# Kernel optimization log

Measured on AMD Instinct MI355X. Metric: run time of the kernel, lower is better.

Reference implementation:

```python
import jax, jax.numpy as jnp
import numpy as np

B, N, GI, GH, GO = 8, 1024, 1024, 128, 128


def _lin_params(k, din, dout):
    # torch.nn.Linear default init: U(-1/sqrt(din), 1/sqrt(din))
    s = 1.0 / np.sqrt(din)
    kw, kb = jax.random.split(k)
    W = jax.random.uniform(kw, (din, dout), jnp.float32, -s, s)
    b = jax.random.uniform(kb, (dout,), jnp.float32, -s, s)
    return W, b


def setup_inputs() -> dict:
    key = jax.random.key(0)
    ks = jax.random.split(key, 6)
    aa_rep = jax.random.normal(ks[0], (B, N, GI), dtype=jnp.float32)
    rpa = jax.random.randint(ks[1], (B, N, N), 0, 2).astype(jnp.int32)
    W_in, b_in = _lin_params(ks[2], GI, GH)
    W_h0, b_h0 = _lin_params(ks[3], GH, GH)
    W_h1, b_h1 = _lin_params(ks[4], GH, GH)
    W_out, b_out = _lin_params(ks[5], GH, GO)
    return dict(aa_rep=aa_rep, rpa=rpa, W_in=W_in, b_in=b_in,
                W_h0=W_h0, b_h0=b_h0, W_h1=W_h1, b_h1=b_h1,
                W_out=W_out, b_out=b_out)


def _norm_adj(rpa):
    # get_graph_edge: edges = nonzero(rpa) minus self-loops; GCNConv then
    # re-adds self-loops and applies symmetric deg^{-1/2} normalization.
    n = rpa.shape[-1]
    A = (rpa != 0).astype(jnp.float32)
    eye = jnp.eye(n, dtype=jnp.float32)
    A = A * (1.0 - eye) + eye  # [B,N,N] A_hat = A (no diag) + I
    deg = A.sum(-1)  # [B,N], includes self-loop
    dinv = jnp.where(deg > 0, 1.0 / jnp.sqrt(deg), 0.0)
    return A * dinv[..., :, None] * dinv[..., None, :]


def reference(aa_rep, rpa, W_in, b_in, W_h0, b_h0, W_h1, b_h1, W_out, b_out):
    Ahat = _norm_adj(rpa)  # [B,N,N]

    def gcn(h, W, b):
        # GCNConv: aggregate(normalized) of (h @ W), then bias; model applies relu
        return jax.nn.relu(jnp.einsum('bij,bjd->bid', Ahat, h @ W) + b)

    h1 = gcn(aa_rep, W_in, b_in)   # layer_in
    h2 = gcn(h1, W_h0, b_h0)       # hidden 0
    h3 = gcn(h2, W_h1, b_h1)       # hidden 1
    h4 = gcn(h3, W_out, b_out)     # layer_out
    # mean over stacked layer outputs reps[1:]
    return (h1 + h2 + h3 + h4) * 0.25
```

## Files before the change

### kernel.cpp

```cpp
#include <hip/hip_runtime.h>
#include <hip/hip_bf16.h>

typedef __bf16 bf16;
typedef __bf16 bf16x4 __attribute__((ext_vector_type(4)));
typedef __bf16 bf16x8 __attribute__((ext_vector_type(8)));
typedef float f32x4 __attribute__((ext_vector_type(4)));

#define NN 1024
#define GH 128
#define MROWS 8192

static __device__ __forceinline__ f32x4 mfma16(bf16x8 a, bf16x8 b, f32x4 c) {
    return __builtin_amdgcn_mfma_f32_16x16x32_bf16(a, b, c, 0, 0, 0);
}

__global__ __launch_bounds__(256) void prep_kernel(
        const int* __restrict__ rpa,
        const float* __restrict__ W0, const float* __restrict__ W1,
        const float* __restrict__ W2, const float* __restrict__ W3,
        unsigned char* __restrict__ A01b, float* __restrict__ dinv,
        bf16* __restrict__ T0, bf16* __restrict__ T1,
        bf16* __restrict__ T2, bf16* __restrict__ T3) {
    int bid = blockIdx.x;
    {
        int rb = (bid & 7) * 256 + (bid >> 3);
        int row  = rb * 4 + (threadIdx.x >> 6);
        int lane = threadIdx.x & 63;
        int i = row & (NN - 1);
        const int4* p = reinterpret_cast<const int4*>(rpa + (size_t)row * NN);
        unsigned char* brow = A01b + (size_t)row * 128;
        int cnt = 0;
#pragma unroll
        for (int it = 0; it < 4; ++it) {
            int4 v = p[lane + it * 64];
            int j = (lane + it * 64) * 4;
            int a0 = (v.x != 0), a1 = (v.y != 0), a2 = (v.z != 0), a3 = (v.w != 0);
            cnt += (a0 & (j + 0 != i)) + (a1 & (j + 1 != i)) +
                   (a2 & (j + 2 != i)) + (a3 & (j + 3 != i));
            unsigned nib = (unsigned)(a0 | (j + 0 == i))
                         | ((unsigned)(a1 | (j + 1 == i)) << 1)
                         | ((unsigned)(a2 | (j + 2 == i)) << 2)
                         | ((unsigned)(a3 | (j + 3 == i)) << 3);
            unsigned pn = __shfl_xor(nib, 1, 64);
            if (!(lane & 1))
                brow[it * 32 + (lane >> 1)] = (unsigned char)(nib | (pn << 4));
        }
#pragma unroll
        for (int off = 32; off > 0; off >>= 1) cnt += __shfl_down(cnt, off, 64);
        if (lane == 0) dinv[row] = rsqrtf((float)(cnt + 1));
    }
    if (threadIdx.x < 11) {
        int t = bid * 11 + threadIdx.x;
        const float* W; bf16* T; int K; int local;
        if (t < 16384)      { W = W0; T = T0; K = NN; local = t; }
        else if (t < 18432) { W = W1; T = T1; K = GH; local = t - 16384; }
        else if (t < 20480) { W = W2; T = T2; K = GH; local = t - 18432; }
        else                { W = W3; T = T3; K = GH; local = t - 20480; }
        int n = local & 127, k0 = (local >> 7) * 8;
        bf16x8 o;
#pragma unroll
        for (int ii = 0; ii < 8; ++ii) o[ii] = (bf16)W[(size_t)(k0 + ii) * GH + n];
        *reinterpret_cast<bf16x8*>(T + (size_t)n * K + k0) = o;
    }
}

__global__ __launch_bounds__(512, 4) void gemm3_kernel(const float* __restrict__ aa,
                                                       const bf16* __restrict__ Wt,
                                                       const float* __restrict__ dinv,
                                                       bf16* __restrict__ Zt) {
    __shared__ bf16 Alds[32768];
    int tid = threadIdx.x;
    int wave = tid >> 6, lane = tid & 63;
    int lrow = lane & 15, lg = lane >> 4;
    int lb = (blockIdx.x & 7) * 32 + (blockIdx.x >> 3);
    int m0 = lb * 32;
#pragma unroll
    for (int i = 0; i < 8; ++i) {
        int idx = i * 512 + tid;
        int row = idx >> 7, u = idx & 127;
        const float* src = aa + (size_t)(m0 + row) * NN + u * 8;
        float4 f0 = *reinterpret_cast<const float4*>(src);
        float4 f1 = *reinterpret_cast<const float4*>(src + 4);
        bf16x8 v;
        v[0] = (bf16)f0.x; v[1] = (bf16)f0.y; v[2] = (bf16)f0.z; v[3] = (bf16)f0.w;
        v[4] = (bf16)f1.x; v[5] = (bf16)f1.y; v[6] = (bf16)f1.z; v[7] = (bf16)f1.w;
        *reinterpret_cast<bf16x8*>(&Alds[(row * 128 + (u ^ (row & 7))) * 8]) = v;
    }
    __syncthreads();
    int c0 = wave * 16;
    const bf16* Bp = Wt + (size_t)(c0 + lrow) * NN + lg * 8;
    f32x4 acc[2][2] = {};
#pragma unroll
    for (int f = 0; f < 32; ++f) {
        bf16x8 bb = *reinterpret_cast<const bf16x8*>(Bp + f * 32);
        int u = f * 4 + lg;
#pragma unroll
        for (int rg = 0; rg < 2; ++rg) {
            int r = rg * 16 + lrow;
            bf16x8 a = *reinterpret_cast<const bf16x8*>(&Alds[(r * 128 + (u ^ (r & 7))) * 8]);
            acc[rg][f & 1] = mfma16(a, bb, acc[rg][f & 1]);
        }
    }
    int rl = lg * 4;
    int col = c0 + lrow;
#pragma unroll
    for (int rg = 0; rg < 2; ++rg) {
        f32x4 s = acc[rg][0] + acc[rg][1];
        int rbase = m0 + rg * 16 + rl;
        float4 d4 = *reinterpret_cast<const float4*>(&dinv[rbase]);
        bf16x4 o;
        o[0] = (bf16)(s[0] * d4.x);
        o[1] = (bf16)(s[1] * d4.y);
        o[2] = (bf16)(s[2] * d4.z);
        o[3] = (bf16)(s[3] * d4.w);
        *reinterpret_cast<bf16x4*>(Zt + (size_t)col * MROWS + rbase) = o;
    }
}

template <int MODE, bool HASW>
__global__ __launch_bounds__(512, 4) void fused3_kernel(const unsigned char* __restrict__ A01b,
                                                        const bf16* __restrict__ Xt,
                                                        const bf16* __restrict__ Wt,
                                                        const float* __restrict__ dinv,
                                                        const float* __restrict__ bias,
                                                        bf16* __restrict__ Hst,
                                                        float* __restrict__ outp) {
    __shared__ bf16 Alds[16384];
    __shared__ bf16 Ths[4096];
    __shared__ bf16 Tls[4096];
    int tid = threadIdx.x;
    int wave = tid >> 6, lane = tid & 63;
    int lrow = lane & 15, lg = lane >> 4;
    int lb = (blockIdx.x & 7) * 32 + (blockIdx.x >> 3);
    int m0 = lb * 32;
    int b = blockIdx.x & 7;
    int c0 = wave * 16;
    const bf16* Bp = Xt + (size_t)(c0 + lrow) * MROWS + b * NN + lg * 8;
    f32x4 acc[2][2] = {};
    int erow = tid >> 4;
    int eub  = (tid & 15) * 4;
    int ers  = erow & 7;
#pragma unroll
    for (int h = 0; h < 2; ++h) {
        if (h) __syncthreads();
        {
            unsigned w = *reinterpret_cast<const unsigned*>(
                A01b + (size_t)(m0 + erow) * 128 + h * 64 + eub);
#pragma unroll
            for (int i = 0; i < 4; ++i) {
                unsigned byte = (w >> (8 * i)) & 0xffu;
                bf16x8 v;
#pragma unroll
                for (int k = 0; k < 8; ++k) v[k] = ((byte >> k) & 1u) ? (bf16)1.f : (bf16)0.f;
                *reinterpret_cast<bf16x8*>(&Alds[(erow * 64 + ((eub + i) ^ ers)) * 8]) = v;
            }
        }
        __syncthreads();
#pragma unroll
        for (int fl = 0; fl < 16; ++fl) {
            int f = h * 16 + fl;
            bf16x8 bb = *reinterpret_cast<const bf16x8*>(Bp + f * 32);
            int ul = fl * 4 + lg;
#pragma unroll
            for (int rg = 0; rg < 2; ++rg) {
                int r = rg * 16 + lrow;
                bf16x8 a = *reinterpret_cast<const bf16x8*>(&Alds[(r * 64 + (ul ^ (r & 7))) * 8]);
                acc[rg][f & 1] = mfma16(a, bb, acc[rg][f & 1]);
            }
        }
    }
    int rl = lg * 4;

    if constexpr (!HASW) {
#pragma unroll
        for (int rg = 0; rg < 2; ++rg) {
            f32x4 s = acc[rg][0] + acc[rg][1];
            int rbase = m0 + rg * 16 + rl;
            float4 d4 = *reinterpret_cast<const float4*>(&dinv[rbase]);
            int col = c0 + lrow;
            float bv = bias[col];
            float v0 = fmaxf(s[0] * d4.x + bv, 0.f);
            float v1 = fmaxf(s[1] * d4.y + bv, 0.f);
            float v2 = fmaxf(s[2] * d4.z + bv, 0.f);
            float v3 = fmaxf(s[3] * d4.w + bv, 0.f);
            float* op = outp + (size_t)rbase * GH + col;
            if (MODE == 0) {
                op[0] = 0.25f * v0; op[GH] = 0.25f * v1;
                op[2 * GH] = 0.25f * v2; op[3 * GH] = 0.25f * v3;
            } else {
                op[0] += 0.25f * v0; op[GH] += 0.25f * v1;
                op[2 * GH] += 0.25f * v2; op[3 * GH] += 0.25f * v3;
            }
            if (MODE != 2) {
                bf16x4 h4;
                h4[0] = (bf16)(v0 * d4.x); h4[1] = (bf16)(v1 * d4.y);
                h4[2] = (bf16)(v2 * d4.z); h4[3] = (bf16)(v3 * d4.w);
                *reinterpret_cast<bf16x4*>(Hst + (size_t)col * MROWS + rbase) = h4;
            }
        }
    } else {
        __syncthreads();
        {
            int tcol = c0 + lrow;
#pragma unroll
            for (int rg = 0; rg < 2; ++rg) {
                f32x4 s = acc[rg][0] + acc[rg][1];
#pragma unroll
                for (int r = 0; r < 4; ++r) {
                    int trow = rg * 16 + rl + r;
                    float tv = s[r];
                    bf16 hi = (bf16)tv;
                    int ei = trow * 128 + (tcol ^ ((trow & 7) << 3));
                    Ths[ei] = hi;
                    Tls[ei] = (bf16)(tv - (float)hi);
                }
            }
        }
        __syncthreads();
        f32x4 u[2] = {};
        int wcol = c0 + lrow;
#pragma unroll
        for (int ks = 0; ks < 4; ++ks) {
            int e0 = ks * 32 + lg * 8;
            bf16x8 wv = *reinterpret_cast<const bf16x8*>(Wt + (size_t)wcol * GH + e0);
#pragma unroll
            for (int rg = 0; rg < 2; ++rg) {
                int trow2 = rg * 16 + lrow;
                int te = trow2 * 128 + (e0 ^ ((trow2 & 7) << 3));
                bf16x8 thi = *reinterpret_cast<const bf16x8*>(&Ths[te]);
                bf16x8 tlo = *reinterpret_cast<const bf16x8*>(&Tls[te]);
                u[rg] = mfma16(thi, wv, u[rg]);
                u[rg] = mfma16(tlo, wv, u[rg]);
            }
        }
#pragma unroll
        for (int rg = 0; rg < 2; ++rg) {
            int rbase = m0 + rg * 16 + rl;
            float4 d4 = *reinterpret_cast<const float4*>(&dinv[rbase]);
            float bv = bias[wcol];
            float v0 = fmaxf(u[rg][0] * d4.x + bv, 0.f);
            float v1 = fmaxf(u[rg][1] * d4.y + bv, 0.f);
            float v2 = fmaxf(u[rg][2] * d4.z + bv, 0.f);
            float v3 = fmaxf(u[rg][3] * d4.w + bv, 0.f);
            float* op = outp + (size_t)rbase * GH + wcol;
            if (MODE == 0) {
                op[0] = 0.25f * v0; op[GH] = 0.25f * v1;
                op[2 * GH] = 0.25f * v2; op[3 * GH] = 0.25f * v3;
            } else {
                op[0] += 0.25f * v0; op[GH] += 0.25f * v1;
                op[2 * GH] += 0.25f * v2; op[3 * GH] += 0.25f * v3;
            }
            if (MODE != 2) {
                bf16x4 h4;
                h4[0] = (bf16)(v0 * d4.x); h4[1] = (bf16)(v1 * d4.y);
                h4[2] = (bf16)(v2 * d4.z); h4[3] = (bf16)(v3 * d4.w);
                *reinterpret_cast<bf16x4*>(Hst + (size_t)wcol * MROWS + rbase) = h4;
            }
        }
    }
}

extern "C" void kernel_launch(void* const* d_in, const int* in_sizes, int n_in,
                              void* d_out, int out_size, void* d_ws, size_t ws_size,
                              hipStream_t stream) {
    const float* aa    = (const float*)d_in[0];
    const int*   rpa   = (const int*)d_in[1];
    const float* W_in  = (const float*)d_in[2];
    const float* b_in  = (const float*)d_in[3];
    const float* W_h0  = (const float*)d_in[4];
    const float* b_h0  = (const float*)d_in[5];
    const float* W_h1  = (const float*)d_in[6];
    const float* b_h1  = (const float*)d_in[7];
    const float* W_out = (const float*)d_in[8];
    const float* b_out = (const float*)d_in[9];
    float* out = (float*)d_out;

    char* ws = (char*)d_ws;
    size_t off = 0;
    float* dinv = (float*)(ws + off); off += (size_t)MROWS * 4;
    unsigned char* A01b = (unsigned char*)(ws + off); off += (size_t)MROWS * 128;
    bf16*  Xt   = (bf16*)(ws + off);  off += (size_t)GH * MROWS * 2;
    bf16*  HstA = (bf16*)(ws + off);  off += (size_t)GH * MROWS * 2;
    bf16*  HstB = (bf16*)(ws + off);  off += (size_t)GH * MROWS * 2;
    bf16*  Wt0  = (bf16*)(ws + off);  off += (size_t)GH * NN * 2;
    bf16*  Wt1  = (bf16*)(ws + off);  off += (size_t)GH * GH * 2;
    bf16*  Wt2  = (bf16*)(ws + off);  off += (size_t)GH * GH * 2;
    bf16*  Wt3  = (bf16*)(ws + off);  off += (size_t)GH * GH * 2;

    prep_kernel<<<2048, 256, 0, stream>>>(rpa, W_in, W_h0, W_h1, W_out,
                                          A01b, dinv, Wt0, Wt1, Wt2, Wt3);
    gemm3_kernel<<<256, 512, 0, stream>>>(aa, Wt0, dinv, Xt);
    fused3_kernel<0, false><<<256, 512, 0, stream>>>(A01b, Xt,   Wt1, dinv, b_in,  HstA, out);
    fused3_kernel<1, true><<<256, 512, 0, stream>>>(A01b, HstA, Wt1, dinv, b_h0, HstB, out);
    fused3_kernel<1, true><<<256, 512, 0, stream>>>(A01b, HstB, Wt2, dinv, b_h1, HstA, out);
    fused3_kernel<2, true><<<256, 512, 0, stream>>>(A01b, HstA, Wt3, dinv, b_out, HstB, out);
}
```

Measured before the change: 75.60 us.

## Enlarge GEMM and fused aggregation tiles to 64 rows with 1024-thread blocks

Both the input GEMM and the fused aggregation kernels now use 1024-thread blocks covering 64 rows, with two row-halves of 8 waves each sharing the same column B-fragments. The K dimension is staged through LDS in four chunks instead of one or two. The redundant barrier before the transform-scratch writes is removed. This roughly halves global B-operand traffic per row, but the grid drops to 128 blocks, which may leave half the CUs idle and adds more barriers per block.

```diff
diff --git a/kernel.cpp b/kernel.cpp
--- a/kernel.cpp
+++ b/kernel.cpp
@@ -64,41 +64,50 @@
     }
 }
 
-__global__ __launch_bounds__(512, 4) void gemm3_kernel(const float* __restrict__ aa,
-                                                       const bf16* __restrict__ Wt,
-                                                       const float* __restrict__ dinv,
-                                                       bf16* __restrict__ Zt) {
-    __shared__ bf16 Alds[32768];
+__global__ __launch_bounds__(1024, 4) void gemm4_kernel(const float* __restrict__ aa,
+                                                        const bf16* __restrict__ Wt,
+                                                        const float* __restrict__ dinv,
+                                                        bf16* __restrict__ Zt) {
+    __shared__ bf16 Alds[16384];
     int tid = threadIdx.x;
     int wave = tid >> 6, lane = tid & 63;
     int lrow = lane & 15, lg = lane >> 4;
-    int lb = (blockIdx.x & 7) * 32 + (blockIdx.x >> 3);
-    int m0 = lb * 32;
-#pragma unroll
-    for (int i = 0; i < 8; ++i) {
-        int idx = i * 512 + tid;
-        int row = idx >> 7, u = idx & 127;
-        const float* src = aa + (size_t)(m0 + row) * NN + u * 8;
-        float4 f0 = *reinterpret_cast<const float4*>(src);
-        float4 f1 = *reinterpret_cast<const float4*>(src + 4);
-        bf16x8 v;
-        v[0] = (bf16)f0.x; v[1] = (bf16)f0.y; v[2] = (bf16)f0.z; v[3] = (bf16)f0.w;
-        v[4] = (bf16)f1.x; v[5] = (bf16)f1.y; v[6] = (bf16)f1.z; v[7] = (bf16)f1.w;
-        *reinterpret_cast<bf16x8*>(&Alds[(row * 128 + (u ^ (row & 7))) * 8]) = v;
-    }
-    __syncthreads();
-    int c0 = wave * 16;
+    int colg = wave & 7, rowh = wave >> 3;
+    int lb = (blockIdx.x & 7) * 16 + (blockIdx.x >> 3);
+    int m0 = lb * 64;
+    int c0 = colg * 16;
     const bf16* Bp = Wt + (size_t)(c0 + lrow) * NN + lg * 8;
     f32x4 acc[2][2] = {};
-#pragma unroll
-    for (int f = 0; f < 32; ++f) {
-        bf16x8 bb = *reinterpret_cast<const bf16x8*>(Bp + f * 32);
-        int u = f * 4 + lg;
-#pragma unroll
-        for (int rg = 0; rg < 2; ++rg) {
-            int r = rg * 16 + lrow;
-            bf16x8 a = *reinterpret_cast<const bf16x8*>(&Alds[(r * 128 + (u ^ (r & 7))) * 8]);
-            acc[rg][f & 1] = mfma16(a, bb, acc[rg][f & 1]);
+    int arow = tid >> 4;
+    int au   = (tid & 15) * 2;
+    int ars  = arow & 7;
+#pragma unroll
+    for (int h = 0; h < 4; ++h) {
+        if (h) __syncthreads();
+        {
+            const float* src = aa + (size_t)(m0 + arow) * NN + h * 256 + au * 8;
+#pragma unroll
+            for (int i = 0; i < 2; ++i) {
+                float4 f0 = *reinterpret_cast<const float4*>(src + i * 8);
+                float4 f1 = *reinterpret_cast<const float4*>(src + i * 8 + 4);
+                bf16x8 v;
+                v[0] = (bf16)f0.x; v[1] = (bf16)f0.y; v[2] = (bf16)f0.z; v[3] = (bf16)f0.w;
+                v[4] = (bf16)f1.x; v[5] = (bf16)f1.y; v[6] = (bf16)f1.z; v[7] = (bf16)f1.w;
+                *reinterpret_cast<bf16x8*>(&Alds[(arow * 32 + ((au + i) ^ ars)) * 8]) = v;
+            }
+        }
+        __syncthreads();
+#pragma unroll
+        for (int fl = 0; fl < 8; ++fl) {
+            int f = h * 8 + fl;
+            bf16x8 bb = *reinterpret_cast<const bf16x8*>(Bp + f * 32);
+            int ul = fl * 4 + lg;
+#pragma unroll
+            for (int rg = 0; rg < 2; ++rg) {
+                int r = rowh * 32 + rg * 16 + lrow;
+                bf16x8 a = *reinterpret_cast<const bf16x8*>(&Alds[(r * 32 + (ul ^ (r & 7))) * 8]);
+                acc[rg][f & 1] = mfma16(a, bb, acc[rg][f & 1]);
+            }
         }
     }
     int rl = lg * 4;
@@ -106,7 +115,7 @@
 #pragma unroll
     for (int rg = 0; rg < 2; ++rg) {
         f32x4 s = acc[rg][0] + acc[rg][1];
-        int rbase = m0 + rg * 16 + rl;
+        int rbase = m0 + rowh * 32 + rg * 16 + rl;
         float4 d4 = *reinterpret_cast<const float4*>(&dinv[rbase]);
         bf16x4 o;
         o[0] = (bf16)(s[0] * d4.x);
@@ -118,53 +127,54 @@
 }
 
 template <int MODE, bool HASW>
-__global__ __launch_bounds__(512, 4) void fused3_kernel(const unsigned char* __restrict__ A01b,
-                                                        const bf16* __restrict__ Xt,
-                                                        const bf16* __restrict__ Wt,
-                                                        const float* __restrict__ dinv,
-                                                        const float* __restrict__ bias,
-                                                        bf16* __restrict__ Hst,
-                                                        float* __restrict__ outp) {
+__global__ __launch_bounds__(1024, 4) void fused4_kernel(const unsigned char* __restrict__ A01b,
+                                                         const bf16* __restrict__ Xt,
+                                                         const bf16* __restrict__ Wt,
+                                                         const float* __restrict__ dinv,
+                                                         const float* __restrict__ bias,
+                                                         bf16* __restrict__ Hst,
+                                                         float* __restrict__ outp) {
     __shared__ bf16 Alds[16384];
-    __shared__ bf16 Ths[4096];
-    __shared__ bf16 Tls[4096];
+    __shared__ bf16 Ths[8192];
+    __shared__ bf16 Tls[8192];
     int tid = threadIdx.x;
     int wave = tid >> 6, lane = tid & 63;
     int lrow = lane & 15, lg = lane >> 4;
-    int lb = (blockIdx.x & 7) * 32 + (blockIdx.x >> 3);
-    int m0 = lb * 32;
+    int colg = wave & 7, rowh = wave >> 3;
+    int lb = (blockIdx.x & 7) * 16 + (blockIdx.x >> 3);
+    int m0 = lb * 64;
     int b = blockIdx.x & 7;
-    int c0 = wave * 16;
+    int c0 = colg * 16;
     const bf16* Bp = Xt + (size_t)(c0 + lrow) * MROWS + b * NN + lg * 8;
     f32x4 acc[2][2] = {};
     int erow = tid >> 4;
-    int eub  = (tid & 15) * 4;
+    int eu2  = (tid & 15) * 2;
     int ers  = erow & 7;
 #pragma unroll
-    for (int h = 0; h < 2; ++h) {
+    for (int h = 0; h < 4; ++h) {
         if (h) __syncthreads();
         {
-            unsigned w = *reinterpret_cast<const unsigned*>(
-                A01b + (size_t)(m0 + erow) * 128 + h * 64 + eub);
-#pragma unroll
-            for (int i = 0; i < 4; ++i) {
+            unsigned short w = *reinterpret_cast<const unsigned short*>(
+                A01b + (size_t)(m0 + erow) * 128 + h * 32 + eu2);
+#pragma unroll
+            for (int i = 0; i < 2; ++i) {
                 unsigned byte = (w >> (8 * i)) & 0xffu;
                 bf16x8 v;
 #pragma unroll
                 for (int k = 0; k < 8; ++k) v[k] = ((byte >> k) & 1u) ? (bf16)1.f : (bf16)0.f;
-                *reinterpret_cast<bf16x8*>(&Alds[(erow * 64 + ((eub + i) ^ ers)) * 8]) = v;
+                *reinterpret_cast<bf16x8*>(&Alds[(erow * 32 + ((eu2 + i) ^ ers)) * 8]) = v;
             }
         }
         __syncthreads();
 #pragma unroll
-        for (int fl = 0; fl < 16; ++fl) {
-            int f = h * 16 + fl;
+        for (int fl = 0; fl < 8; ++fl) {
+            int f = h * 8 + fl;
             bf16x8 bb = *reinterpret_cast<const bf16x8*>(Bp + f * 32);
             int ul = fl * 4 + lg;
 #pragma unroll
             for (int rg = 0; rg < 2; ++rg) {
-                int r = rg * 16 + lrow;
-                bf16x8 a = *reinterpret_cast<const bf16x8*>(&Alds[(r * 64 + (ul ^ (r & 7))) * 8]);
+                int r = rowh * 32 + rg * 16 + lrow;
+                bf16x8 a = *reinterpret_cast<const bf16x8*>(&Alds[(r * 32 + (ul ^ (r & 7))) * 8]);
                 acc[rg][f & 1] = mfma16(a, bb, acc[rg][f & 1]);
             }
         }
@@ -172,12 +182,12 @@
     int rl = lg * 4;
 
     if constexpr (!HASW) {
+        int col = c0 + lrow;
 #pragma unroll
         for (int rg = 0; rg < 2; ++rg) {
             f32x4 s = acc[rg][0] + acc[rg][1];
-            int rbase = m0 + rg * 16 + rl;
+            int rbase = m0 + rowh * 32 + rg * 16 + rl;
             float4 d4 = *reinterpret_cast<const float4*>(&dinv[rbase]);
-            int col = c0 + lrow;
             float bv = bias[col];
             float v0 = fmaxf(s[0] * d4.x + bv, 0.f);
             float v1 = fmaxf(s[1] * d4.y + bv, 0.f);
@@ -199,7 +209,6 @@
             }
         }
     } else {
-        __syncthreads();
         {
             int tcol = c0 + lrow;
 #pragma unroll
@@ -207,7 +216,7 @@
                 f32x4 s = acc[rg][0] + acc[rg][1];
 #pragma unroll
                 for (int r = 0; r < 4; ++r) {
-                    int trow = rg * 16 + rl + r;
+                    int trow = rowh * 32 + rg * 16 + rl + r;
                     float tv = s[r];
                     bf16 hi = (bf16)tv;
                     int ei = trow * 128 + (tcol ^ ((trow & 7) << 3));
@@ -225,7 +234,7 @@
             bf16x8 wv = *reinterpret_cast<const bf16x8*>(Wt + (size_t)wcol * GH + e0);
 #pragma unroll
             for (int rg = 0; rg < 2; ++rg) {
-                int trow2 = rg * 16 + lrow;
+                int trow2 = rowh * 32 + rg * 16 + lrow;
                 int te = trow2 * 128 + (e0 ^ ((trow2 & 7) << 3));
                 bf16x8 thi = *reinterpret_cast<const bf16x8*>(&Ths[te]);
                 bf16x8 tlo = *reinterpret_cast<const bf16x8*>(&Tls[te]);
@@ -235,7 +244,7 @@
         }
 #pragma unroll
         for (int rg = 0; rg < 2; ++rg) {
-            int rbase = m0 + rg * 16 + rl;
+            int rbase = m0 + rowh * 32 + rg * 16 + rl;
             float4 d4 = *reinterpret_cast<const float4*>(&dinv[rbase]);
             float bv = bias[wcol];
             float v0 = fmaxf(u[rg][0] * d4.x + bv, 0.f);
@@ -289,9 +298,9 @@
 
     prep_kernel<<<2048, 256, 0, stream>>>(rpa, W_in, W_h0, W_h1, W_out,
                                           A01b, dinv, Wt0, Wt1, Wt2, Wt3);
-    gemm3_kernel<<<256, 512, 0, stream>>>(aa, Wt0, dinv, Xt);
-    fused3_kernel<0, false><<<256, 512, 0, stream>>>(A01b, Xt,   Wt1, dinv, b_in,  HstA, out);
-    fused3_kernel<1, true><<<256, 512, 0, stream>>>(A01b, HstA, Wt1, dinv, b_h0, HstB, out);
-    fused3_kernel<1, true><<<256, 512, 0, stream>>>(A01b, HstB, Wt2, dinv, b_h1, HstA, out);
-    fused3_kernel<2, true><<<256, 512, 0, stream>>>(A01b, HstA, Wt3, dinv, b_out, HstB, out);
-}
+    gemm4_kernel<<<128, 1024, 0, stream>>>(aa, Wt0, dinv, Xt);
+    fused4_kernel<0, false><<<128, 1024, 0, stream>>>(A01b, Xt,   Wt1, dinv, b_in,  HstA, out);
+    fused4_kernel<1, true><<<128, 1024, 0, stream>>>(A01b, HstA, Wt1, dinv, b_h0, HstB, out);
+    fused4_kernel<1, true><<<128, 1024, 0, stream>>>(A01b, HstB, Wt2, dinv, b_h1, HstA, out);
+    fused4_kernel<2, true><<<128, 1024, 0, stream>>>(A01b, HstA, Wt3, dinv, b_out, HstB, out);
+}
```

Result: slower. 122.4 us (+61.9%).

## Merge adjacency prep with first GEMM and fold dinv scaling into aggregation

Applied to the files above, without the earlier changes.

Splits the W_in transpose into its own small kernel, then fuses the adjacency bit-packing and degree computation with the aa@W_in GEMM in a single launch. Because the GEMM no longer waits on dinv, the column dinv scaling moves into the first aggregation kernel, where the adjacency tile is built with dinv values instead of ones. This removes one dependency and lets the memory-bound rpa scan overlap with the GEMM. The cost is an extra tiny launch, extra dinv loads in the first aggregation, and a different bf16 rounding point.

```diff
diff --git a/kernel.cpp b/kernel.cpp
--- a/kernel.cpp
+++ b/kernel.cpp
@@ -14,18 +14,29 @@
     return __builtin_amdgcn_mfma_f32_16x16x32_bf16(a, b, c, 0, 0, 0);
 }
 
-__global__ __launch_bounds__(256) void prep_kernel(
-        const int* __restrict__ rpa,
-        const float* __restrict__ W0, const float* __restrict__ W1,
-        const float* __restrict__ W2, const float* __restrict__ W3,
+__global__ __launch_bounds__(256) void wtrans0_kernel(const float* __restrict__ W0,
+                                                      bf16* __restrict__ T0) {
+    int t = blockIdx.x * 256 + threadIdx.x;
+    int n = t & 127, k0 = (t >> 7) * 8;
+    bf16x8 o;
+#pragma unroll
+    for (int ii = 0; ii < 8; ++ii) o[ii] = (bf16)W0[(size_t)(k0 + ii) * GH + n];
+    *reinterpret_cast<bf16x8*>(T0 + (size_t)n * NN + k0) = o;
+}
+
+__global__ __launch_bounds__(512, 4) void prep_gemm_kernel(
+        const int* __restrict__ rpa, const float* __restrict__ aa,
+        const float* __restrict__ W1, const float* __restrict__ W2, const float* __restrict__ W3,
+        const bf16* __restrict__ Wt0,
         unsigned char* __restrict__ A01b, float* __restrict__ dinv,
-        bf16* __restrict__ T0, bf16* __restrict__ T1,
-        bf16* __restrict__ T2, bf16* __restrict__ T3) {
-    int bid = blockIdx.x;
-    {
-        int rb = (bid & 7) * 256 + (bid >> 3);
-        int row  = rb * 4 + (threadIdx.x >> 6);
-        int lane = threadIdx.x & 63;
+        bf16* __restrict__ T1, bf16* __restrict__ T2, bf16* __restrict__ T3,
+        bf16* __restrict__ Yt) {
+    __shared__ bf16 Alds[32768];
+    int bid = blockIdx.x, tid = threadIdx.x;
+    if (bid < 1024) {
+        int rb = (bid & 7) * 128 + (bid >> 3);
+        int wave = tid >> 6, lane = tid & 63;
+        int row = rb * 8 + wave;
         int i = row & (NN - 1);
         const int4* p = reinterpret_cast<const int4*>(rpa + (size_t)row * NN);
         unsigned char* brow = A01b + (size_t)row * 128;
@@ -48,76 +59,65 @@
 #pragma unroll
         for (int off = 32; off > 0; off >>= 1) cnt += __shfl_down(cnt, off, 64);
         if (lane == 0) dinv[row] = rsqrtf((float)(cnt + 1));
+        if (tid < 6) {
+            int t = bid * 6 + tid;
+            const float* W; bf16* T; int local;
+            if (t < 2048)      { W = W1; T = T1; local = t; }
+            else if (t < 4096) { W = W2; T = T2; local = t - 2048; }
+            else               { W = W3; T = T3; local = t - 4096; }
+            int n = local & 127, k0 = (local >> 7) * 8;
+            bf16x8 o;
+#pragma unroll
+            for (int ii = 0; ii < 8; ++ii) o[ii] = (bf16)W[(size_t)(k0 + ii) * GH + n];
+            *reinterpret_cast<bf16x8*>(T + (size_t)n * GH + k0) = o;
+        }
+    } else {
+        int g = bid - 1024;
+        int wave = tid >> 6, lane = tid & 63;
+        int lrow = lane & 15, lg = lane >> 4;
+        int lb = (g & 7) * 32 + (g >> 3);
+        int m0 = lb * 32;
+#pragma unroll
+        for (int i = 0; i < 8; ++i) {
+            int idx = i * 512 + tid;
+            int row = idx >> 7, u = idx & 127;
+            const float* src = aa + (size_t)(m0 + row) * NN + u * 8;
+            float4 f0 = *reinterpret_cast<const float4*>(src);
+            float4 f1 = *reinterpret_cast<const float4*>(src + 4);
+            bf16x8 v;
+            v[0] = (bf16)f0.x; v[1] = (bf16)f0.y; v[2] = (bf16)f0.z; v[3] = (bf16)f0.w;
+            v[4] = (bf16)f1.x; v[5] = (bf16)f1.y; v[6] = (bf16)f1.z; v[7] = (bf16)f1.w;
+            *reinterpret_cast<bf16x8*>(&Alds[(row * 128 + (u ^ (row & 7))) * 8]) = v;
+        }
+        __syncthreads();
+        int c0 = wave * 16;
+        const bf16* Bp = Wt0 + (size_t)(c0 + lrow) * NN + lg * 8;
+        f32x4 acc[2][2] = {};
+#pragma unroll
+        for (int f = 0; f < 32; ++f) {
+            bf16x8 bb = *reinterpret_cast<const bf16x8*>(Bp + f * 32);
+            int u = f * 4 + lg;
+#pragma unroll
+            for (int rg = 0; rg < 2; ++rg) {
+                int r = rg * 16 + lrow;
+                bf16x8 a = *reinterpret_cast<const bf16x8*>(&Alds[(r * 128 + (u ^ (r & 7))) * 8]);
+                acc[rg][f & 1] = mfma16(a, bb, acc[rg][f & 1]);
+            }
+        }
+        int rl = lg * 4;
+        int col = c0 + lrow;
+#pragma unroll
+        for (int rg = 0; rg < 2; ++rg) {
+            f32x4 s = acc[rg][0] + acc[rg][1];
+            int rbase = m0 + rg * 16 + rl;
+            bf16x4 o;
+            o[0] = (bf16)s[0]; o[1] = (bf16)s[1]; o[2] = (bf16)s[2]; o[3] = (bf16)s[3];
+            *reinterpret_cast<bf16x4*>(Yt + (size_t)col * MROWS + rbase) = o;
+        }
     }
-    if (threadIdx.x < 11) {
-        int t = bid * 11 + threadIdx.x;
-        const float* W; bf16* T; int K; int local;
-        if (t < 16384)      { W = W0; T = T0; K = NN; local = t; }
-        else if (t < 18432) { W = W1; T = T1; K = GH; local = t - 16384; }
-        else if (t < 20480) { W = W2; T = T2; K = GH; local = t - 18432; }
-        else                { W = W3; T = T3; K = GH; local = t - 20480; }
-        int n = local & 127, k0 = (local >> 7) * 8;
-        bf16x8 o;
-#pragma unroll
-        for (int ii = 0; ii < 8; ++ii) o[ii] = (bf16)W[(size_t)(k0 + ii) * GH + n];
-        *reinterpret_cast<bf16x8*>(T + (size_t)n * K + k0) = o;
-    }
-}
-
-__global__ __launch_bounds__(512, 4) void gemm3_kernel(const float* __restrict__ aa,
-                                                       const bf16* __restrict__ Wt,
-                                                       const float* __restrict__ dinv,
-                                                       bf16* __restrict__ Zt) {
-    __shared__ bf16 Alds[32768];
-    int tid = threadIdx.x;
-    int wave = tid >> 6, lane = tid & 63;
-    int lrow = lane & 15, lg = lane >> 4;
-    int lb = (blockIdx.x & 7) * 32 + (blockIdx.x >> 3);
-    int m0 = lb * 32;
-#pragma unroll
-    for (int i = 0; i < 8; ++i) {
-        int idx = i * 512 + tid;
-        int row = idx >> 7, u = idx & 127;
-        const float* src = aa + (size_t)(m0 + row) * NN + u * 8;
-        float4 f0 = *reinterpret_cast<const float4*>(src);
-        float4 f1 = *reinterpret_cast<const float4*>(src + 4);
-        bf16x8 v;
-        v[0] = (bf16)f0.x; v[1] = (bf16)f0.y; v[2] = (bf16)f0.z; v[3] = (bf16)f0.w;
-        v[4] = (bf16)f1.x; v[5] = (bf16)f1.y; v[6] = (bf16)f1.z; v[7] = (bf16)f1.w;
-        *reinterpret_cast<bf16x8*>(&Alds[(row * 128 + (u ^ (row & 7))) * 8]) = v;
-    }
-    __syncthreads();
-    int c0 = wave * 16;
-    const bf16* Bp = Wt + (size_t)(c0 + lrow) * NN + lg * 8;
-    f32x4 acc[2][2] = {};
-#pragma unroll
-    for (int f = 0; f < 32; ++f) {
-        bf16x8 bb = *reinterpret_cast<const bf16x8*>(Bp + f * 32);
-        int u = f * 4 + lg;
-#pragma unroll
-        for (int rg = 0; rg < 2; ++rg) {
-            int r = rg * 16 + lrow;
-            bf16x8 a = *reinterpret_cast<const bf16x8*>(&Alds[(r * 128 + (u ^ (r & 7))) * 8]);
-            acc[rg][f & 1] = mfma16(a, bb, acc[rg][f & 1]);
-        }
-    }
-    int rl = lg * 4;
-    int col = c0 + lrow;
-#pragma unroll
-    for (int rg = 0; rg < 2; ++rg) {
-        f32x4 s = acc[rg][0] + acc[rg][1];
-        int rbase = m0 + rg * 16 + rl;
-        float4 d4 = *reinterpret_cast<const float4*>(&dinv[rbase]);
-        bf16x4 o;
-        o[0] = (bf16)(s[0] * d4.x);
-        o[1] = (bf16)(s[1] * d4.y);
-        o[2] = (bf16)(s[2] * d4.z);
-        o[3] = (bf16)(s[3] * d4.w);
-        *reinterpret_cast<bf16x4*>(Zt + (size_t)col * MROWS + rbase) = o;
-    }
-}
-
-template <int MODE, bool HASW>
+}
+
+template <int MODE, bool HASW, bool DSCALE>
 __global__ __launch_bounds__(512, 4) void fused3_kernel(const unsigned char* __restrict__ A01b,
                                                         const bf16* __restrict__ Xt,
                                                         const bf16* __restrict__ Wt,
@@ -150,8 +150,22 @@
             for (int i = 0; i < 4; ++i) {
                 unsigned byte = (w >> (8 * i)) & 0xffu;
                 bf16x8 v;
-#pragma unroll
-                for (int k = 0; k < 8; ++k) v[k] = ((byte >> k) & 1u) ? (bf16)1.f : (bf16)0.f;
+                if constexpr (DSCALE) {
+                    const float* dq = dinv + b * NN + (h * 64 + eub + i) * 8;
+                    float4 q0 = *reinterpret_cast<const float4*>(dq);
+                    float4 q1 = *reinterpret_cast<const float4*>(dq + 4);
+                    v[0] = (byte & 1u)   ? (bf16)q0.x : (bf16)0.f;
+                    v[1] = (byte & 2u)   ? (bf16)q0.y : (bf16)0.f;
+                    v[2] = (byte & 4u)   ? (bf16)q0.z : (bf16)0.f;
+                    v[3] = (byte & 8u)   ? (bf16)q0.w : (bf16)0.f;
+                    v[4] = (byte & 16u)  ? (bf16)q1.x : (bf16)0.f;
+                    v[5] = (byte & 32u)  ? (bf16)q1.y : (bf16)0.f;
+                    v[6] = (byte & 64u)  ? (bf16)q1.z : (bf16)0.f;
+                    v[7] = (byte & 128u) ? (bf16)q1.w : (bf16)0.f;
+                } else {
+#pragma unroll
+                    for (int k = 0; k < 8; ++k) v[k] = ((byte >> k) & 1u) ? (bf16)1.f : (bf16)0.f;
+                }
                 *reinterpret_cast<bf16x8*>(&Alds[(erow * 64 + ((eub + i) ^ ers)) * 8]) = v;
             }
         }
@@ -279,7 +293,7 @@
     size_t off = 0;
     float* dinv = (float*)(ws + off); off += (size_t)MROWS * 4;
     unsigned char* A01b = (unsigned char*)(ws + off); off += (size_t)MROWS * 128;
-    bf16*  Xt   = (bf16*)(ws + off);  off += (size_t)GH * MROWS * 2;
+    bf16*  Yt   = (bf16*)(ws + off);  off += (size_t)GH * MROWS * 2;
     bf16*  HstA = (bf16*)(ws + off);  off += (size_t)GH * MROWS * 2;
     bf16*  HstB = (bf16*)(ws + off);  off += (size_t)GH * MROWS * 2;
     bf16*  Wt0  = (bf16*)(ws + off);  off += (size_t)GH * NN * 2;
@@ -287,11 +301,11 @@
     bf16*  Wt2  = (bf16*)(ws + off);  off += (size_t)GH * GH * 2;
     bf16*  Wt3  = (bf16*)(ws + off);  off += (size_t)GH * GH * 2;
 
-    prep_kernel<<<2048, 256, 0, stream>>>(rpa, W_in, W_h0, W_h1, W_out,
-                                          A01b, dinv, Wt0, Wt1, Wt2, Wt3);
-    gemm3_kernel<<<256, 512, 0, stream>>>(aa, Wt0, dinv, Xt);
-    fused3_kernel<0, false><<<256, 512, 0, stream>>>(A01b, Xt,   Wt1, dinv, b_in,  HstA, out);
-    fused3_kernel<1, true><<<256, 512, 0, stream>>>(A01b, HstA, Wt1, dinv, b_h0, HstB, out);
-    fused3_kernel<1, true><<<256, 512, 0, stream>>>(A01b, HstB, Wt2, dinv, b_h1, HstA, out);
-    fused3_kernel<2, true><<<256, 512, 0, stream>>>(A01b, HstA, Wt3, dinv, b_out, HstB, out);
-}
+    wtrans0_kernel<<<64, 256, 0, stream>>>(W_in, Wt0);
+    prep_gemm_kernel<<<1280, 512, 0, stream>>>(rpa, aa, W_h0, W_h1, W_out, Wt0,
+                                               A01b, dinv, Wt1, Wt2, Wt3, Yt);
+    fused3_kernel<0, false, true><<<256, 512, 0, stream>>>(A01b, Yt,   Wt1, dinv, b_in,  HstA, out);
+    fused3_kernel<1, true, false><<<256, 512, 0, stream>>>(A01b, HstA, Wt1, dinv, b_h0, HstB, out);
+    fused3_kernel<1, true, false><<<256, 512, 0, stream>>>(A01b, HstB, Wt2, dinv, b_h1, HstA, out);
+    fused3_kernel<2, true, false><<<256, 512, 0, stream>>>(A01b, HstA, Wt3, dinv, b_out, HstB, out);
+}
```

New measurement: 88.70 us. 1.17x slower.
